# Kernel optimization log

Hardware: AMD Instinct MI355X
Metric: run time of the kernel (lower is better)

Reference implementation:

```python
import jax, jax.numpy as jnp
import numpy as np

N, E, IN, ED, H, C, G, NC = 50000, 800000, 128, 32, 4, 16, 64, 2
HC = H * C  # 64
NEG_SLOPE = 0.2
EPS = 1e-5


def _layernorm(x, g, b):
    mu = jnp.mean(x, axis=-1, keepdims=True)
    var = jnp.mean((x - mu) ** 2, axis=-1, keepdims=True)
    return (x - mu) * jax.lax.rsqrt(var + EPS) * g + b


def _gat(x, src, dst, edge_attr, W, a_src, a_dst, We, a_edge, b):
    """PyG GATConv (v1) with edge features, concat=True."""
    n = x.shape[0]
    h, c = a_src.shape
    xw = (x @ W).reshape(n, h, c)                       # [N,H,C]
    al_src = jnp.sum(xw * a_src, axis=-1)               # [N,H]
    al_dst = jnp.sum(xw * a_dst, axis=-1)               # [N,H]
    ew = (edge_attr @ We).reshape(-1, h, c)             # [Ef,H,C]
    al_e = jnp.sum(ew * a_edge, axis=-1)                # [Ef,H]
    alpha = al_src[src] + al_dst[dst] + al_e            # [Ef,H]
    alpha = jnp.where(alpha > 0, alpha, NEG_SLOPE * alpha)
    # segment softmax over incoming edges of each dst node
    amax = jax.ops.segment_max(alpha, dst, num_segments=n)
    amax = jnp.where(jnp.isfinite(amax), amax, 0.0)
    ex = jnp.exp(alpha - amax[dst])
    denom = jax.ops.segment_sum(ex, dst, num_segments=n)
    att = ex / (denom[dst] + 1e-16)                     # [Ef,H]
    msg = xw[src] * att[:, :, None]                     # [Ef,H,C]
    out = jax.ops.segment_sum(msg, dst, num_segments=n) # [N,H,C]
    return out.reshape(n, h * c) + b


def setup_inputs() -> dict:
    ks = jax.random.split(jax.random.key(0), 24)
    s = 0.1
    inp = {
        "x": jax.random.normal(ks[0], (N, IN), jnp.float32),
        "edge_attr": jax.random.normal(ks[1], (E, ED), jnp.float32),
        "W1": jax.random.normal(ks[2], (IN, HC), jnp.float32) * s,
        "as1": jax.random.normal(ks[3], (H, C), jnp.float32) * s,
        "ad1": jax.random.normal(ks[4], (H, C), jnp.float32) * s,
        "We1": jax.random.normal(ks[5], (ED, HC), jnp.float32) * s,
        "ae1": jax.random.normal(ks[6], (H, C), jnp.float32) * s,
        "b1": jnp.zeros((HC,), jnp.float32),
        "W2": jax.random.normal(ks[7], (HC, HC), jnp.float32) * s,
        "as2": jax.random.normal(ks[8], (H, C), jnp.float32) * s,
        "ad2": jax.random.normal(ks[9], (H, C), jnp.float32) * s,
        "We2": jax.random.normal(ks[10], (ED, HC), jnp.float32) * s,
        "ae2": jax.random.normal(ks[11], (H, C), jnp.float32) * s,
        "b2": jnp.zeros((HC,), jnp.float32),
        "g1": jnp.ones((HC,), jnp.float32),
        "be1": jnp.zeros((HC,), jnp.float32),
        "fw1": jax.random.normal(ks[12], (HC, 32), jnp.float32) * s,
        "fb1": jnp.zeros((32,), jnp.float32),
        "g2": jnp.ones((32,), jnp.float32),
        "be2": jnp.zeros((32,), jnp.float32),
        "fw2": jax.random.normal(ks[13], (32, NC), jnp.float32) * s,
        "fb2": jnp.zeros((NC,), jnp.float32),
        "edge_index": jax.random.randint(ks[14], (2, E), 0, N, jnp.int64),
        "batch": jnp.sort(jax.random.randint(ks[15], (N,), 0, G, jnp.int64)),
    }
    return inp


def reference(x, edge_attr, W1, as1, ad1, We1, ae1, b1, W2, as2, ad2, We2, ae2,
              b2, g1, be1, fw1, fb1, g2, be2, fw2, fb2, edge_index, batch):
    src, dst = edge_index[0], edge_index[1]
    e = edge_attr.shape[0]
    # add_self_loops with fill_value='mean' (mean of incoming edge_attr per node)
    cnt = jax.ops.segment_sum(jnp.ones((e,), x.dtype), dst, num_segments=N)
    loop_ea = jax.ops.segment_sum(edge_attr, dst, num_segments=N) / jnp.clip(cnt, 1.0)[:, None]
    ar = jnp.arange(N)
    src_f = jnp.concatenate([src, ar])
    dst_f = jnp.concatenate([dst, ar])
    ea_f = jnp.concatenate([edge_attr, loop_ea], axis=0)

    h = _gat(x, src_f, dst_f, ea_f, W1, as1, ad1, We1, ae1, b1)
    h = jax.nn.relu(h)
    h = _layernorm(h, g1, be1)
    h = _gat(h, src_f, dst_f, ea_f, W2, as2, ad2, We2, ae2, b2)
    h = jax.nn.relu(h)
    pooled = jax.ops.segment_max(h, batch, num_segments=G)   # global_max_pool
    pooled = jnp.where(jnp.isfinite(pooled), pooled, 0.0)
    z = pooled @ fw1 + fb1
    z = _layernorm(z, g2, be2)
    z = jax.nn.relu(z)
    # dropout(p=0.4) is identity in eval mode
    z = z @ fw2 + fb2
    return jax.nn.log_softmax(z, axis=1)
```

## Files before the change

### kernel.cpp

```cpp
#include <hip/hip_runtime.h>
#include <math.h>

#define N_NODES 50000
#define N_EDGES 800000
#define IN_DIM 128
#define ED_DIM 32
#define NH 4
#define CH 16
#define HC 64
#define NG 64
#define NCL 2
#define NEG_SLOPE 0.2f
#define LN_EPS 1e-5f
#define NBLK1 196
#define NB_TILE 3125
#define NB_ECH 3125

__global__ void k_scan_local(const int* __restrict__ cnt, int* __restrict__ tmp_ex,
                             int* __restrict__ bsum) {
    __shared__ int sd[256];
    int t = threadIdx.x, idx = blockIdx.x * 256 + t;
    int v = (idx < N_NODES) ? cnt[idx] : 0;
    sd[t] = v; __syncthreads();
    for (int off = 1; off < 256; off <<= 1) {
        int add = (t >= off) ? sd[t - off] : 0;
        __syncthreads();
        sd[t] += add;
        __syncthreads();
    }
    if (idx < N_NODES) tmp_ex[idx] = sd[t] - v;
    if (t == 255) bsum[blockIdx.x] = sd[t];
}

__global__ __launch_bounds__(256) void k_phase1(
        const float* __restrict__ X, const float* __restrict__ W,
        const float* __restrict__ AS, const float* __restrict__ AD,
        float* __restrict__ XW, float* __restrict__ ALS, float* __restrict__ ALD,
        const float* __restrict__ ea,
        const float* __restrict__ We1, const float* __restrict__ ae1,
        const float* __restrict__ We2, const float* __restrict__ ae2,
        float4* __restrict__ ale8,
        const int* __restrict__ dst, int* __restrict__ cnt, int* __restrict__ rank_e) {
    __shared__ float smem[IN_DIM * HC + 16 * IN_DIM];
    int job = blockIdx.x % 3;
    int bid = blockIdx.x / 3;
    int t = threadIdx.x;
    if (job == 0) {
        const int K = IN_DIM;
        float* sW = smem;
        float* sX = smem + K * HC;
        for (int i = t; i < K * HC; i += 256) sW[i] = W[i];
        int nb = bid * 16;
        for (int i = t; i < 16 * K; i += 256) sX[i] = X[(long long)nb * K + i];
        __syncthreads();
        int sub = t >> 6, j = t & 63;
        float acc[4] = {0.f, 0.f, 0.f, 0.f};
        #pragma unroll 8
        for (int k = 0; k < K; ++k) {
            float wv = sW[k * HC + j];
            #pragma unroll
            for (int q = 0; q < 4; ++q) acc[q] += sX[(sub + 4 * q) * K + k] * wv;
        }
        float as_ = AS[j], ad_ = AD[j];
        #pragma unroll
        for (int q = 0; q < 4; ++q) {
            int n = nb + sub + 4 * q;
            XW[(long long)n * HC + j] = acc[q];
            float vs = acc[q] * as_, vd = acc[q] * ad_;
            #pragma unroll
            for (int m = 1; m < 16; m <<= 1) { vs += __shfl_xor(vs, m); vd += __shfl_xor(vd, m); }
            if ((j & 15) == 0) {
                int h = j >> 4;
                ALS[n * 4 + h] = vs; ALD[n * 4 + h] = vd;
            }
        }
    } else if (job == 1) {
        float* sVe = smem;
        {
            int d = t >> 3, k = t & 7;
            int l = k >> 2, h = k & 3;
            const float* We = l ? We2 : We1;
            const float* ae = l ? ae2 : ae1;
            float s = 0.f;
            #pragma unroll
            for (int c = 0; c < CH; ++c) s += We[d * HC + h * CH + c] * ae[h * CH + c];
            sVe[d * 8 + k] = s;
        }
        __syncthreads();
        int e = bid * 256 + t;
        if (e >= N_EDGES) return;
        float a[8];
        #pragma unroll
        for (int k = 0; k < 8; ++k) a[k] = 0.f;
        const float4* er4 = (const float4*)(ea + (long long)e * ED_DIM);
        #pragma unroll
        for (int q = 0; q < ED_DIM / 4; ++q) {
            float4 v = er4[q];
            float ev[4] = {v.x, v.y, v.z, v.w};
            #pragma unroll
            for (int u = 0; u < 4; ++u) {
                #pragma unroll
                for (int k = 0; k < 8; ++k) a[k] += ev[u] * sVe[(q * 4 + u) * 8 + k];
            }
        }
        float4* out = ale8 + (long long)e * 2;
        out[0] = make_float4(a[0], a[1], a[2], a[3]);
        out[1] = make_float4(a[4], a[5], a[6], a[7]);
    } else {
        int e = bid * 256 + t;
        if (e < N_EDGES) rank_e[e] = atomicAdd(&cnt[dst[e]], 1);
    }
}

__global__ void k_scan_perm(const int* __restrict__ tmp_ex, const int* __restrict__ bsum,
                            int* __restrict__ row_start,
                            const int* __restrict__ dst, const int* __restrict__ srcI,
                            const int* __restrict__ rank_e, int2* __restrict__ perm_src) {
    __shared__ int sd[256];
    __shared__ int sboff[256];
    int t = threadIdx.x;
    int v = (t < NBLK1) ? bsum[t] : 0;
    sd[t] = v; __syncthreads();
    for (int off = 1; off < 256; off <<= 1) {
        int add = (t >= off) ? sd[t - off] : 0;
        __syncthreads();
        sd[t] += add;
        __syncthreads();
    }
    sboff[t] = sd[t] - v;
    __syncthreads();
    if (blockIdx.x < NBLK1) {
        int idx = blockIdx.x * 256 + t;
        if (idx < N_NODES) row_start[idx] = tmp_ex[idx] + sboff[blockIdx.x];
        if (idx == 0) row_start[N_NODES] = N_EDGES;
    } else {
        int e = (blockIdx.x - NBLK1) * 256 + t;
        if (e < N_EDGES) {
            int d = dst[e];
            int pos = tmp_ex[d] + sboff[d >> 8] + rank_e[e];
            perm_src[pos] = make_int2(e, srcI[e]);
        }
    }
}

template<int K>
__global__ void k_xw(const float* __restrict__ X, const float* __restrict__ W,
                     const float* __restrict__ AS, const float* __restrict__ AD,
                     float* __restrict__ XW, float* __restrict__ ALS, float* __restrict__ ALD) {
    __shared__ float sW[K * HC];
    __shared__ float sX[16 * K];
    int t = threadIdx.x;
    for (int i = t; i < K * HC; i += 256) sW[i] = W[i];
    int nb = blockIdx.x * 16;
    for (int i = t; i < 16 * K; i += 256) sX[i] = X[(long long)nb * K + i];
    __syncthreads();
    int sub = t >> 6, j = t & 63;
    float acc[4] = {0.f, 0.f, 0.f, 0.f};
    #pragma unroll 8
    for (int k = 0; k < K; ++k) {
        float wv = sW[k * HC + j];
        #pragma unroll
        for (int q = 0; q < 4; ++q) acc[q] += sX[(sub + 4 * q) * K + k] * wv;
    }
    float as_ = AS[j], ad_ = AD[j];
    #pragma unroll
    for (int q = 0; q < 4; ++q) {
        int n = nb + sub + 4 * q;
        XW[(long long)n * HC + j] = acc[q];
        float vs = acc[q] * as_, vd = acc[q] * ad_;
        #pragma unroll
        for (int m = 1; m < 16; m <<= 1) { vs += __shfl_xor(vs, m); vd += __shfl_xor(vd, m); }
        if ((j & 15) == 0) {
            int h = j >> 4;
            ALS[n * 4 + h] = vs; ALD[n * 4 + h] = vd;
        }
    }
}

template<bool DO_LN, int LOFF>
__global__ void k_agg(const int* __restrict__ rs, const int2* __restrict__ ps,
                      const float* __restrict__ ale8,
                      const float* __restrict__ ALS, const float* __restrict__ ALD,
                      const float* __restrict__ XW, const float* __restrict__ bias,
                      const float* __restrict__ gam, const float* __restrict__ bet,
                      float* __restrict__ OUT) {
    int n = (blockIdx.x * blockDim.x + threadIdx.x) >> 6;
    if (n >= N_NODES) return;
    int lane = threadIdx.x & 63;
    int h = lane >> 4;
    int e0 = rs[n], e1 = rs[n + 1];
    float adn = ALD[n * 4 + h];
    float acc0 = 0.f, l0 = 0.f, as0 = 0.f;
    float acc1 = 0.f, l1 = 0.f, as1 = 0.f;
    float acc2 = 0.f, l2 = 0.f, as2 = 0.f;
    float acc3 = 0.f, l3 = 0.f, as3 = 0.f;
    int e = e0;
    for (; e + 3 < e1; e += 4) {
        int2 pA = ps[e], pB = ps[e + 1], pC = ps[e + 2], pD = ps[e + 3];
        float aeA = ale8[(long long)pA.x * 8 + LOFF + h];
        float aeB = ale8[(long long)pB.x * 8 + LOFF + h];
        float aeC = ale8[(long long)pC.x * 8 + LOFF + h];
        float aeD = ale8[(long long)pD.x * 8 + LOFF + h];
        float xA = XW[pA.y * HC + lane];
        float xB = XW[pB.y * HC + lane];
        float xC = XW[pC.y * HC + lane];
        float xD = XW[pD.y * HC + lane];
        float aA = ALS[pA.y * 4 + h] + adn + aeA;
        float aB = ALS[pB.y * 4 + h] + adn + aeB;
        float aC = ALS[pC.y * 4 + h] + adn + aeC;
        float aD = ALS[pD.y * 4 + h] + adn + aeD;
        aA = aA > 0.f ? aA : NEG_SLOPE * aA;
        aB = aB > 0.f ? aB : NEG_SLOPE * aB;
        aC = aC > 0.f ? aC : NEG_SLOPE * aC;
        aD = aD > 0.f ? aD : NEG_SLOPE * aD;
        float qA = __expf(aA), qB = __expf(aB), qC = __expf(aC), qD = __expf(aD);
        acc0 += qA * xA; l0 += qA; as0 += aeA;
        acc1 += qB * xB; l1 += qB; as1 += aeB;
        acc2 += qC * xC; l2 += qC; as2 += aeC;
        acc3 += qD * xD; l3 += qD; as3 += aeD;
    }
    for (; e < e1; ++e) {
        int2 pA = ps[e];
        float aeA = ale8[(long long)pA.x * 8 + LOFF + h];
        float xA = XW[pA.y * HC + lane];
        float aA = ALS[pA.y * 4 + h] + adn + aeA;
        aA = aA > 0.f ? aA : NEG_SLOPE * aA;
        float qA = __expf(aA);
        acc0 += qA * xA; l0 += qA; as0 += aeA;
    }
    int d = e1 - e0;
    float invd = 1.f / (float)(d > 0 ? d : 1);
    float aSelf = ALS[n * 4 + h] + adn + (as0 + as1 + as2 + as3) * invd;
    aSelf = aSelf > 0.f ? aSelf : NEG_SLOPE * aSelf;
    float pS = __expf(aSelf);
    float acc = (acc0 + acc1) + (acc2 + acc3) + pS * XW[n * HC + lane];
    float l = (l0 + l1) + (l2 + l3) + pS;
    float v = acc / (l + 1e-16f) + bias[lane];
    v = fmaxf(v, 0.f);
    if (DO_LN) {
        float s1 = v;
        #pragma unroll
        for (int mm = 1; mm < 64; mm <<= 1) s1 += __shfl_xor(s1, mm);
        float mean = s1 * (1.f / 64.f);
        float dd = v - mean;
        float s2 = dd * dd;
        #pragma unroll
        for (int mm = 1; mm < 64; mm <<= 1) s2 += __shfl_xor(s2, mm);
        float var = s2 * (1.f / 64.f);
        v = dd * rsqrtf(var + LN_EPS) * gam[lane] + bet[lane];
    }
    OUT[(long long)n * HC + lane] = v;
}

__global__ void k_pool(const float* __restrict__ H2, const int* __restrict__ batch,
                       float* __restrict__ pooled) {
    int j = threadIdx.x & 63;
    int r = threadIdx.x >> 6;
    int base = blockIdx.x * 128;
    int gcur = -1; float rm = 0.f;
    for (int n = base + r; n < base + 128 && n < N_NODES; n += 4) {
        int g = batch[n];
        if (g != gcur) {
            if (gcur >= 0) atomicMax((unsigned int*)&pooled[gcur * HC + j], __float_as_uint(rm));
            gcur = g; rm = 0.f;
        }
        rm = fmaxf(rm, H2[(long long)n * HC + j]);
    }
    if (gcur >= 0) atomicMax((unsigned int*)&pooled[gcur * HC + j], __float_as_uint(rm));
}

__global__ void k_head(const float* __restrict__ pooled,
                       const float* __restrict__ fw1, const float* __restrict__ fb1,
                       const float* __restrict__ g2, const float* __restrict__ be2,
                       const float* __restrict__ fw2, const float* __restrict__ fb2,
                       float* __restrict__ out) {
    int g = blockIdx.x;
    int j = threadIdx.x;
    float z = 0.f;
    if (j < 32) {
        for (int k = 0; k < HC; ++k) z += pooled[g * HC + k] * fw1[k * 32 + j];
        z += fb1[j];
    }
    float s1 = (j < 32) ? z : 0.f;
    for (int m = 1; m < 32; m <<= 1) s1 += __shfl_xor(s1, m, 32);
    float mean = s1 * (1.f / 32.f);
    float d = z - mean;
    float s2 = (j < 32) ? d * d : 0.f;
    for (int m = 1; m < 32; m <<= 1) s2 += __shfl_xor(s2, m, 32);
    float var = s2 * (1.f / 32.f);
    float zz = 0.f;
    if (j < 32) {
        zz = d * rsqrtf(var + LN_EPS) * g2[j] + be2[j];
        zz = fmaxf(zz, 0.f);
    }
    float p0 = (j < 32) ? zz * fw2[j * NCL + 0] : 0.f;
    float p1 = (j < 32) ? zz * fw2[j * NCL + 1] : 0.f;
    for (int m = 1; m < 32; m <<= 1) { p0 += __shfl_xor(p0, m, 32); p1 += __shfl_xor(p1, m, 32); }
    if (j == 0) {
        float l0 = p0 + fb2[0], l1 = p1 + fb2[1];
        float mx = fmaxf(l0, l1);
        float ls = mx + logf(__expf(l0 - mx) + __expf(l1 - mx));
        out[g * NCL + 0] = l0 - ls;
        out[g * NCL + 1] = l1 - ls;
    }
}

extern "C" void kernel_launch(void* const* d_in, const int* in_sizes, int n_in,
                              void* d_out, int out_size, void* d_ws, size_t ws_size,
                              hipStream_t stream) {
    const float* x   = (const float*)d_in[0];
    const float* ea  = (const float*)d_in[1];
    const float* W1  = (const float*)d_in[2];
    const float* as1 = (const float*)d_in[3];
    const float* ad1 = (const float*)d_in[4];
    const float* We1 = (const float*)d_in[5];
    const float* ae1 = (const float*)d_in[6];
    const float* b1  = (const float*)d_in[7];
    const float* W2  = (const float*)d_in[8];
    const float* as2 = (const float*)d_in[9];
    const float* ad2 = (const float*)d_in[10];
    const float* We2 = (const float*)d_in[11];
    const float* ae2 = (const float*)d_in[12];
    const float* b2  = (const float*)d_in[13];
    const float* g1  = (const float*)d_in[14];
    const float* be1 = (const float*)d_in[15];
    const float* fw1 = (const float*)d_in[16];
    const float* fb1 = (const float*)d_in[17];
    const float* g2  = (const float*)d_in[18];
    const float* be2 = (const float*)d_in[19];
    const float* fw2 = (const float*)d_in[20];
    const float* fb2 = (const float*)d_in[21];
    const int* eidx  = (const int*)d_in[22];
    const int* batch = (const int*)d_in[23];
    const int* srcI = eidx;
    const int* dstI = eidx + N_EDGES;

    char* w = (char*)d_ws;
    auto alloc = [&](size_t bytes) { char* p = w; w += (bytes + 255) & ~(size_t)255; return p; };
    int*   cnt       = (int*)  alloc((size_t)N_NODES * 4);
    int*   row_start = (int*)  alloc((size_t)(N_NODES + 1) * 4);
    int*   rank_e    = (int*)  alloc((size_t)N_EDGES * 4);
    int*   tmp_ex    = (int*)  alloc((size_t)N_NODES * 4);
    int*   bsum      = (int*)  alloc(256 * 4);
    int2*  perm_src  = (int2*) alloc((size_t)N_EDGES * 8);
    float4* ale8     = (float4*)alloc((size_t)N_EDGES * 32);
    float* xw1       = (float*)alloc((size_t)N_NODES * HC * 4);
    float* als1      = (float*)alloc((size_t)N_NODES * 4 * 4);
    float* ald1      = (float*)alloc((size_t)N_NODES * 4 * 4);
    float* h1        = (float*)alloc((size_t)N_NODES * HC * 4);
    float* als2      = (float*)alloc((size_t)N_NODES * 4 * 4);
    float* ald2      = (float*)alloc((size_t)N_NODES * 4 * 4);
    float* pooled    = (float*)alloc((size_t)NG * HC * 4);
    float* xw2 = xw1;
    float* h2  = h1;

    hipMemsetAsync(cnt, 0, (size_t)N_NODES * 4, stream);
    hipMemsetAsync(pooled, 0, (size_t)NG * HC * 4, stream);

    k_phase1<<<3 * NB_TILE, 256, 0, stream>>>(x, W1, as1, ad1, xw1, als1, ald1,
                                              ea, We1, ae1, We2, ae2, ale8,
                                              dstI, cnt, rank_e);
    k_scan_local<<<NBLK1, 256, 0, stream>>>(cnt, tmp_ex, bsum);
    k_scan_perm<<<NBLK1 + NB_ECH, 256, 0, stream>>>(tmp_ex, bsum, row_start,
                                                    dstI, srcI, rank_e, perm_src);

    k_agg<true, 0><<<N_NODES / 4, 256, 0, stream>>>(row_start, perm_src, (const float*)ale8,
                                                    als1, ald1, xw1, b1, g1, be1, h1);
    k_xw<HC><<<N_NODES / 16, 256, 0, stream>>>(h1, W2, as2, ad2, xw2, als2, ald2);
    k_agg<false, 4><<<N_NODES / 4, 256, 0, stream>>>(row_start, perm_src, (const float*)ale8,
                                                     als2, ald2, xw2, b2, nullptr, nullptr, h2);

    k_pool<<<(N_NODES + 127) / 128, 256, 0, stream>>>(h2, batch, pooled);
    k_head<<<NG, 64, 0, stream>>>(pooled, fw1, fb1, g2, be2, fw2, fb2, (float*)d_out);
}
```

Measured before the change: 418.6 us.

## Fuse layer-2 projection into layer-1 aggregation and pooling into layer-2 aggregation

The layer-1 aggregation kernel now applies LayerNorm, stages the normalized row in shared memory and multiplies it by W2 in place, writing XW2 and the layer-2 attention logits directly. The separate h1 buffer and k_xw launch go away. The layer-2 aggregation then does global max pooling itself with per-node atomicMax into pooled, which removes the h2 write/read and the k_pool launch. In exchange it issues many more atomics, one per node and lane instead of one per run of nodes, and W2 is read from global/L1 per node instead of from a shared tile.

```diff
diff --git a/kernel.cpp b/kernel.cpp
--- a/kernel.cpp
+++ b/kernel.cpp
@@ -143,47 +143,17 @@
     }
 }
 
-template<int K>
-__global__ void k_xw(const float* __restrict__ X, const float* __restrict__ W,
-                     const float* __restrict__ AS, const float* __restrict__ AD,
-                     float* __restrict__ XW, float* __restrict__ ALS, float* __restrict__ ALD) {
-    __shared__ float sW[K * HC];
-    __shared__ float sX[16 * K];
-    int t = threadIdx.x;
-    for (int i = t; i < K * HC; i += 256) sW[i] = W[i];
-    int nb = blockIdx.x * 16;
-    for (int i = t; i < 16 * K; i += 256) sX[i] = X[(long long)nb * K + i];
-    __syncthreads();
-    int sub = t >> 6, j = t & 63;
-    float acc[4] = {0.f, 0.f, 0.f, 0.f};
-    #pragma unroll 8
-    for (int k = 0; k < K; ++k) {
-        float wv = sW[k * HC + j];
-        #pragma unroll
-        for (int q = 0; q < 4; ++q) acc[q] += sX[(sub + 4 * q) * K + k] * wv;
-    }
-    float as_ = AS[j], ad_ = AD[j];
-    #pragma unroll
-    for (int q = 0; q < 4; ++q) {
-        int n = nb + sub + 4 * q;
-        XW[(long long)n * HC + j] = acc[q];
-        float vs = acc[q] * as_, vd = acc[q] * ad_;
-        #pragma unroll
-        for (int m = 1; m < 16; m <<= 1) { vs += __shfl_xor(vs, m); vd += __shfl_xor(vd, m); }
-        if ((j & 15) == 0) {
-            int h = j >> 4;
-            ALS[n * 4 + h] = vs; ALD[n * 4 + h] = vd;
-        }
-    }
-}
-
-template<bool DO_LN, int LOFF>
-__global__ void k_agg(const int* __restrict__ rs, const int2* __restrict__ ps,
-                      const float* __restrict__ ale8,
-                      const float* __restrict__ ALS, const float* __restrict__ ALD,
-                      const float* __restrict__ XW, const float* __restrict__ bias,
-                      const float* __restrict__ gam, const float* __restrict__ bet,
-                      float* __restrict__ OUT) {
+__global__ void k_agg1x(const int* __restrict__ rs, const int2* __restrict__ ps,
+                        const float* __restrict__ ale8,
+                        const float* __restrict__ ALS, const float* __restrict__ ALD,
+                        const float* __restrict__ XW, const float* __restrict__ bias,
+                        const float* __restrict__ gam, const float* __restrict__ bet,
+                        const float* __restrict__ W2,
+                        const float* __restrict__ AS2, const float* __restrict__ AD2,
+                        float* __restrict__ XW2, float* __restrict__ ALS2,
+                        float* __restrict__ ALD2) {
+    __shared__ float sh[4][HC];
+    int wid = threadIdx.x >> 6;
     int n = (blockIdx.x * blockDim.x + threadIdx.x) >> 6;
     if (n >= N_NODES) return;
     int lane = threadIdx.x & 63;
@@ -197,10 +167,10 @@
     int e = e0;
     for (; e + 3 < e1; e += 4) {
         int2 pA = ps[e], pB = ps[e + 1], pC = ps[e + 2], pD = ps[e + 3];
-        float aeA = ale8[(long long)pA.x * 8 + LOFF + h];
-        float aeB = ale8[(long long)pB.x * 8 + LOFF + h];
-        float aeC = ale8[(long long)pC.x * 8 + LOFF + h];
-        float aeD = ale8[(long long)pD.x * 8 + LOFF + h];
+        float aeA = ale8[(long long)pA.x * 8 + h];
+        float aeB = ale8[(long long)pB.x * 8 + h];
+        float aeC = ale8[(long long)pC.x * 8 + h];
+        float aeD = ale8[(long long)pD.x * 8 + h];
         float xA = XW[pA.y * HC + lane];
         float xB = XW[pB.y * HC + lane];
         float xC = XW[pC.y * HC + lane];
@@ -221,7 +191,7 @@
     }
     for (; e < e1; ++e) {
         int2 pA = ps[e];
-        float aeA = ale8[(long long)pA.x * 8 + LOFF + h];
+        float aeA = ale8[(long long)pA.x * 8 + h];
         float xA = XW[pA.y * HC + lane];
         float aA = ALS[pA.y * 4 + h] + adn + aeA;
         aA = aA > 0.f ? aA : NEG_SLOPE * aA;
@@ -237,7 +207,7 @@
     float l = (l0 + l1) + (l2 + l3) + pS;
     float v = acc / (l + 1e-16f) + bias[lane];
     v = fmaxf(v, 0.f);
-    if (DO_LN) {
+    {
         float s1 = v;
         #pragma unroll
         for (int mm = 1; mm < 64; mm <<= 1) s1 += __shfl_xor(s1, mm);
@@ -249,24 +219,82 @@
         float var = s2 * (1.f / 64.f);
         v = dd * rsqrtf(var + LN_EPS) * gam[lane] + bet[lane];
     }
-    OUT[(long long)n * HC + lane] = v;
-}
-
-__global__ void k_pool(const float* __restrict__ H2, const int* __restrict__ batch,
-                       float* __restrict__ pooled) {
-    int j = threadIdx.x & 63;
-    int r = threadIdx.x >> 6;
-    int base = blockIdx.x * 128;
-    int gcur = -1; float rm = 0.f;
-    for (int n = base + r; n < base + 128 && n < N_NODES; n += 4) {
-        int g = batch[n];
-        if (g != gcur) {
-            if (gcur >= 0) atomicMax((unsigned int*)&pooled[gcur * HC + j], __float_as_uint(rm));
-            gcur = g; rm = 0.f;
-        }
-        rm = fmaxf(rm, H2[(long long)n * HC + j]);
-    }
-    if (gcur >= 0) atomicMax((unsigned int*)&pooled[gcur * HC + j], __float_as_uint(rm));
+    sh[wid][lane] = v;
+    __syncthreads();
+    float a2 = 0.f;
+    #pragma unroll 8
+    for (int k = 0; k < HC; ++k) {
+        a2 += sh[wid][k] * W2[k * HC + lane];
+    }
+    XW2[(long long)n * HC + lane] = a2;
+    float vs = a2 * AS2[lane], vd = a2 * AD2[lane];
+    #pragma unroll
+    for (int m = 1; m < 16; m <<= 1) { vs += __shfl_xor(vs, m); vd += __shfl_xor(vd, m); }
+    if ((lane & 15) == 0) {
+        ALS2[n * 4 + h] = vs; ALD2[n * 4 + h] = vd;
+    }
+}
+
+__global__ void k_agg2p(const int* __restrict__ rs, const int2* __restrict__ ps,
+                        const float* __restrict__ ale8,
+                        const float* __restrict__ ALS, const float* __restrict__ ALD,
+                        const float* __restrict__ XW, const float* __restrict__ bias,
+                        const int* __restrict__ batch, float* __restrict__ pooled) {
+    int n = (blockIdx.x * blockDim.x + threadIdx.x) >> 6;
+    if (n >= N_NODES) return;
+    int lane = threadIdx.x & 63;
+    int h = lane >> 4;
+    int e0 = rs[n], e1 = rs[n + 1];
+    float adn = ALD[n * 4 + h];
+    float acc0 = 0.f, l0 = 0.f, as0 = 0.f;
+    float acc1 = 0.f, l1 = 0.f, as1 = 0.f;
+    float acc2 = 0.f, l2 = 0.f, as2 = 0.f;
+    float acc3 = 0.f, l3 = 0.f, as3 = 0.f;
+    int e = e0;
+    for (; e + 3 < e1; e += 4) {
+        int2 pA = ps[e], pB = ps[e + 1], pC = ps[e + 2], pD = ps[e + 3];
+        float aeA = ale8[(long long)pA.x * 8 + 4 + h];
+        float aeB = ale8[(long long)pB.x * 8 + 4 + h];
+        float aeC = ale8[(long long)pC.x * 8 + 4 + h];
+        float aeD = ale8[(long long)pD.x * 8 + 4 + h];
+        float xA = XW[pA.y * HC + lane];
+        float xB = XW[pB.y * HC + lane];
+        float xC = XW[pC.y * HC + lane];
+        float xD = XW[pD.y * HC + lane];
+        float aA = ALS[pA.y * 4 + h] + adn + aeA;
+        float aB = ALS[pB.y * 4 + h] + adn + aeB;
+        float aC = ALS[pC.y * 4 + h] + adn + aeC;
+        float aD = ALS[pD.y * 4 + h] + adn + aeD;
+        aA = aA > 0.f ? aA : NEG_SLOPE * aA;
+        aB = aB > 0.f ? aB : NEG_SLOPE * aB;
+        aC = aC > 0.f ? aC : NEG_SLOPE * aC;
+        aD = aD > 0.f ? aD : NEG_SLOPE * aD;
+        float qA = __expf(aA), qB = __expf(aB), qC = __expf(aC), qD = __expf(aD);
+        acc0 += qA * xA; l0 += qA; as0 += aeA;
+        acc1 += qB * xB; l1 += qB; as1 += aeB;
+        acc2 += qC * xC; l2 += qC; as2 += aeC;
+        acc3 += qD * xD; l3 += qD; as3 += aeD;
+    }
+    for (; e < e1; ++e) {
+        int2 pA = ps[e];
+        float aeA = ale8[(long long)pA.x * 8 + 4 + h];
+        float xA = XW[pA.y * HC + lane];
+        float aA = ALS[pA.y * 4 + h] + adn + aeA;
+        aA = aA > 0.f ? aA : NEG_SLOPE * aA;
+        float qA = __expf(aA);
+        acc0 += qA * xA; l0 += qA; as0 += aeA;
+    }
+    int d = e1 - e0;
+    float invd = 1.f / (float)(d > 0 ? d : 1);
+    float aSelf = ALS[n * 4 + h] + adn + (as0 + as1 + as2 + as3) * invd;
+    aSelf = aSelf > 0.f ? aSelf : NEG_SLOPE * aSelf;
+    float pS = __expf(aSelf);
+    float acc = (acc0 + acc1) + (acc2 + acc3) + pS * XW[n * HC + lane];
+    float l = (l0 + l1) + (l2 + l3) + pS;
+    float v = acc / (l + 1e-16f) + bias[lane];
+    v = fmaxf(v, 0.f);
+    int g = batch[n];
+    atomicMax((unsigned int*)&pooled[g * HC + lane], __float_as_uint(v));
 }
 
 __global__ void k_head(const float* __restrict__ pooled,
@@ -347,12 +375,10 @@
     float* xw1       = (float*)alloc((size_t)N_NODES * HC * 4);
     float* als1      = (float*)alloc((size_t)N_NODES * 4 * 4);
     float* ald1      = (float*)alloc((size_t)N_NODES * 4 * 4);
-    float* h1        = (float*)alloc((size_t)N_NODES * HC * 4);
+    float* xw2       = (float*)alloc((size_t)N_NODES * HC * 4);
     float* als2      = (float*)alloc((size_t)N_NODES * 4 * 4);
     float* ald2      = (float*)alloc((size_t)N_NODES * 4 * 4);
     float* pooled    = (float*)alloc((size_t)NG * HC * 4);
-    float* xw2 = xw1;
-    float* h2  = h1;
 
     hipMemsetAsync(cnt, 0, (size_t)N_NODES * 4, stream);
     hipMemsetAsync(pooled, 0, (size_t)NG * HC * 4, stream);
@@ -364,12 +390,11 @@
     k_scan_perm<<<NBLK1 + NB_ECH, 256, 0, stream>>>(tmp_ex, bsum, row_start,
                                                     dstI, srcI, rank_e, perm_src);
 
-    k_agg<true, 0><<<N_NODES / 4, 256, 0, stream>>>(row_start, perm_src, (const float*)ale8,
-                                                    als1, ald1, xw1, b1, g1, be1, h1);
-    k_xw<HC><<<N_NODES / 16, 256, 0, stream>>>(h1, W2, as2, ad2, xw2, als2, ald2);
-    k_agg<false, 4><<<N_NODES / 4, 256, 0, stream>>>(row_start, perm_src, (const float*)ale8,
-                                                     als2, ald2, xw2, b2, nullptr, nullptr, h2);
-
-    k_pool<<<(N_NODES + 127) / 128, 256, 0, stream>>>(h2, batch, pooled);
+    k_agg1x<<<N_NODES / 4, 256, 0, stream>>>(row_start, perm_src, (const float*)ale8,
+                                             als1, ald1, xw1, b1, g1, be1,
+                                             W2, as2, ad2, xw2, als2, ald2);
+    k_agg2p<<<N_NODES / 4, 256, 0, stream>>>(row_start, perm_src, (const float*)ale8,
+                                             als2, ald2, xw2, b2, batch, pooled);
+
     k_head<<<NG, 64, 0, stream>>>(pooled, fw1, fb1, g2, be2, fw2, fb2, (float*)d_out);
 }
```

Measured after the change: 435.4 us. 1.04x slower.

## Pack source attention logits beside XW rows and use persistent aggregation waves

Applied to the files above, without the earlier changes.

Stores each node's per-head source attention logit in a padded 68-float row right after its 64 XW features. Each gathered edge then reads its features and logit from the same row, where before it touched a separate ALS array. The aggregation kernels also change to a grid-stride loop over a fixed 2048 blocks instead of one wave per node, which cuts launch and wave scheduling overhead. The cost is a larger, non-power-of-two row stride that may misalign rows against cache lines, and persistent waves can load-balance worse across skewed degree distributions.

```diff
diff --git a/kernel.cpp b/kernel.cpp
--- a/kernel.cpp
+++ b/kernel.cpp
@@ -8,6 +8,7 @@
 #define NH 4
 #define CH 16
 #define HC 64
+#define XS 68
 #define NG 64
 #define NCL 2
 #define NEG_SLOPE 0.2f
@@ -15,6 +16,8 @@
 #define NBLK1 196
 #define NB_TILE 3125
 #define NB_ECH 3125
+#define AGG_BLOCKS 2048
+#define AGG_WAVES (AGG_BLOCKS * 4)
 
 __global__ void k_scan_local(const int* __restrict__ cnt, int* __restrict__ tmp_ex,
                              int* __restrict__ bsum) {
@@ -35,7 +38,7 @@
 __global__ __launch_bounds__(256) void k_phase1(
         const float* __restrict__ X, const float* __restrict__ W,
         const float* __restrict__ AS, const float* __restrict__ AD,
-        float* __restrict__ XW, float* __restrict__ ALS, float* __restrict__ ALD,
+        float* __restrict__ XWA, float* __restrict__ ALD,
         const float* __restrict__ ea,
         const float* __restrict__ We1, const float* __restrict__ ae1,
         const float* __restrict__ We2, const float* __restrict__ ae2,
@@ -65,13 +68,14 @@
         #pragma unroll
         for (int q = 0; q < 4; ++q) {
             int n = nb + sub + 4 * q;
-            XW[(long long)n * HC + j] = acc[q];
+            XWA[(long long)n * XS + j] = acc[q];
             float vs = acc[q] * as_, vd = acc[q] * ad_;
             #pragma unroll
             for (int m = 1; m < 16; m <<= 1) { vs += __shfl_xor(vs, m); vd += __shfl_xor(vd, m); }
             if ((j & 15) == 0) {
                 int h = j >> 4;
-                ALS[n * 4 + h] = vs; ALD[n * 4 + h] = vd;
+                XWA[(long long)n * XS + 64 + h] = vs;
+                ALD[n * 4 + h] = vd;
             }
         }
     } else if (job == 1) {
@@ -146,7 +150,7 @@
 template<int K>
 __global__ void k_xw(const float* __restrict__ X, const float* __restrict__ W,
                      const float* __restrict__ AS, const float* __restrict__ AD,
-                     float* __restrict__ XW, float* __restrict__ ALS, float* __restrict__ ALD) {
+                     float* __restrict__ XWA, float* __restrict__ ALD) {
     __shared__ float sW[K * HC];
     __shared__ float sX[16 * K];
     int t = threadIdx.x;
@@ -166,13 +170,14 @@
     #pragma unroll
     for (int q = 0; q < 4; ++q) {
         int n = nb + sub + 4 * q;
-        XW[(long long)n * HC + j] = acc[q];
+        XWA[(long long)n * XS + j] = acc[q];
         float vs = acc[q] * as_, vd = acc[q] * ad_;
         #pragma unroll
         for (int m = 1; m < 16; m <<= 1) { vs += __shfl_xor(vs, m); vd += __shfl_xor(vd, m); }
         if ((j & 15) == 0) {
             int h = j >> 4;
-            ALS[n * 4 + h] = vs; ALD[n * 4 + h] = vd;
+            XWA[(long long)n * XS + 64 + h] = vs;
+            ALD[n * 4 + h] = vd;
         }
     }
 }
@@ -180,76 +185,77 @@
 template<bool DO_LN, int LOFF>
 __global__ void k_agg(const int* __restrict__ rs, const int2* __restrict__ ps,
                       const float* __restrict__ ale8,
-                      const float* __restrict__ ALS, const float* __restrict__ ALD,
-                      const float* __restrict__ XW, const float* __restrict__ bias,
+                      const float* __restrict__ XWA, const float* __restrict__ ALD,
+                      const float* __restrict__ bias,
                       const float* __restrict__ gam, const float* __restrict__ bet,
                       float* __restrict__ OUT) {
-    int n = (blockIdx.x * blockDim.x + threadIdx.x) >> 6;
-    if (n >= N_NODES) return;
+    int gw = (blockIdx.x * blockDim.x + threadIdx.x) >> 6;
     int lane = threadIdx.x & 63;
     int h = lane >> 4;
-    int e0 = rs[n], e1 = rs[n + 1];
-    float adn = ALD[n * 4 + h];
-    float acc0 = 0.f, l0 = 0.f, as0 = 0.f;
-    float acc1 = 0.f, l1 = 0.f, as1 = 0.f;
-    float acc2 = 0.f, l2 = 0.f, as2 = 0.f;
-    float acc3 = 0.f, l3 = 0.f, as3 = 0.f;
-    int e = e0;
-    for (; e + 3 < e1; e += 4) {
-        int2 pA = ps[e], pB = ps[e + 1], pC = ps[e + 2], pD = ps[e + 3];
-        float aeA = ale8[(long long)pA.x * 8 + LOFF + h];
-        float aeB = ale8[(long long)pB.x * 8 + LOFF + h];
-        float aeC = ale8[(long long)pC.x * 8 + LOFF + h];
-        float aeD = ale8[(long long)pD.x * 8 + LOFF + h];
-        float xA = XW[pA.y * HC + lane];
-        float xB = XW[pB.y * HC + lane];
-        float xC = XW[pC.y * HC + lane];
-        float xD = XW[pD.y * HC + lane];
-        float aA = ALS[pA.y * 4 + h] + adn + aeA;
-        float aB = ALS[pB.y * 4 + h] + adn + aeB;
-        float aC = ALS[pC.y * 4 + h] + adn + aeC;
-        float aD = ALS[pD.y * 4 + h] + adn + aeD;
-        aA = aA > 0.f ? aA : NEG_SLOPE * aA;
-        aB = aB > 0.f ? aB : NEG_SLOPE * aB;
-        aC = aC > 0.f ? aC : NEG_SLOPE * aC;
-        aD = aD > 0.f ? aD : NEG_SLOPE * aD;
-        float qA = __expf(aA), qB = __expf(aB), qC = __expf(aC), qD = __expf(aD);
-        acc0 += qA * xA; l0 += qA; as0 += aeA;
-        acc1 += qB * xB; l1 += qB; as1 += aeB;
-        acc2 += qC * xC; l2 += qC; as2 += aeC;
-        acc3 += qD * xD; l3 += qD; as3 += aeD;
-    }
-    for (; e < e1; ++e) {
-        int2 pA = ps[e];
-        float aeA = ale8[(long long)pA.x * 8 + LOFF + h];
-        float xA = XW[pA.y * HC + lane];
-        float aA = ALS[pA.y * 4 + h] + adn + aeA;
-        aA = aA > 0.f ? aA : NEG_SLOPE * aA;
-        float qA = __expf(aA);
-        acc0 += qA * xA; l0 += qA; as0 += aeA;
-    }
-    int d = e1 - e0;
-    float invd = 1.f / (float)(d > 0 ? d : 1);
-    float aSelf = ALS[n * 4 + h] + adn + (as0 + as1 + as2 + as3) * invd;
-    aSelf = aSelf > 0.f ? aSelf : NEG_SLOPE * aSelf;
-    float pS = __expf(aSelf);
-    float acc = (acc0 + acc1) + (acc2 + acc3) + pS * XW[n * HC + lane];
-    float l = (l0 + l1) + (l2 + l3) + pS;
-    float v = acc / (l + 1e-16f) + bias[lane];
-    v = fmaxf(v, 0.f);
-    if (DO_LN) {
-        float s1 = v;
-        #pragma unroll
-        for (int mm = 1; mm < 64; mm <<= 1) s1 += __shfl_xor(s1, mm);
-        float mean = s1 * (1.f / 64.f);
-        float dd = v - mean;
-        float s2 = dd * dd;
-        #pragma unroll
-        for (int mm = 1; mm < 64; mm <<= 1) s2 += __shfl_xor(s2, mm);
-        float var = s2 * (1.f / 64.f);
-        v = dd * rsqrtf(var + LN_EPS) * gam[lane] + bet[lane];
-    }
-    OUT[(long long)n * HC + lane] = v;
+    for (int n = gw; n < N_NODES; n += AGG_WAVES) {
+        int e0 = rs[n], e1 = rs[n + 1];
+        float adn = ALD[n * 4 + h];
+        float acc0 = 0.f, l0 = 0.f, as0 = 0.f;
+        float acc1 = 0.f, l1 = 0.f, as1 = 0.f;
+        float acc2 = 0.f, l2 = 0.f, as2 = 0.f;
+        float acc3 = 0.f, l3 = 0.f, as3 = 0.f;
+        int e = e0;
+        for (; e + 3 < e1; e += 4) {
+            int2 pA = ps[e], pB = ps[e + 1], pC = ps[e + 2], pD = ps[e + 3];
+            float aeA = ale8[(long long)pA.x * 8 + LOFF + h];
+            float aeB = ale8[(long long)pB.x * 8 + LOFF + h];
+            float aeC = ale8[(long long)pC.x * 8 + LOFF + h];
+            float aeD = ale8[(long long)pD.x * 8 + LOFF + h];
+            float xA = XWA[(long long)pA.y * XS + lane];
+            float xB = XWA[(long long)pB.y * XS + lane];
+            float xC = XWA[(long long)pC.y * XS + lane];
+            float xD = XWA[(long long)pD.y * XS + lane];
+            float aA = XWA[(long long)pA.y * XS + 64 + h] + adn + aeA;
+            float aB = XWA[(long long)pB.y * XS + 64 + h] + adn + aeB;
+            float aC = XWA[(long long)pC.y * XS + 64 + h] + adn + aeC;
+            float aD = XWA[(long long)pD.y * XS + 64 + h] + adn + aeD;
+            aA = aA > 0.f ? aA : NEG_SLOPE * aA;
+            aB = aB > 0.f ? aB : NEG_SLOPE * aB;
+            aC = aC > 0.f ? aC : NEG_SLOPE * aC;
+            aD = aD > 0.f ? aD : NEG_SLOPE * aD;
+            float qA = __expf(aA), qB = __expf(aB), qC = __expf(aC), qD = __expf(aD);
+            acc0 += qA * xA; l0 += qA; as0 += aeA;
+            acc1 += qB * xB; l1 += qB; as1 += aeB;
+            acc2 += qC * xC; l2 += qC; as2 += aeC;
+            acc3 += qD * xD; l3 += qD; as3 += aeD;
+        }
+        for (; e < e1; ++e) {
+            int2 pA = ps[e];
+            float aeA = ale8[(long long)pA.x * 8 + LOFF + h];
+            float xA = XWA[(long long)pA.y * XS + lane];
+            float aA = XWA[(long long)pA.y * XS + 64 + h] + adn + aeA;
+            aA = aA > 0.f ? aA : NEG_SLOPE * aA;
+            float qA = __expf(aA);
+            acc0 += qA * xA; l0 += qA; as0 += aeA;
+        }
+        int d = e1 - e0;
+        float invd = 1.f / (float)(d > 0 ? d : 1);
+        float aSelf = XWA[(long long)n * XS + 64 + h] + adn + (as0 + as1 + as2 + as3) * invd;
+        aSelf = aSelf > 0.f ? aSelf : NEG_SLOPE * aSelf;
+        float pS = __expf(aSelf);
+        float acc = (acc0 + acc1) + (acc2 + acc3) + pS * XWA[(long long)n * XS + lane];
+        float l = (l0 + l1) + (l2 + l3) + pS;
+        float v = acc / (l + 1e-16f) + bias[lane];
+        v = fmaxf(v, 0.f);
+        if (DO_LN) {
+            float s1 = v;
+            #pragma unroll
+            for (int mm = 1; mm < 64; mm <<= 1) s1 += __shfl_xor(s1, mm);
+            float mean = s1 * (1.f / 64.f);
+            float dd = v - mean;
+            float s2 = dd * dd;
+            #pragma unroll
+            for (int mm = 1; mm < 64; mm <<= 1) s2 += __shfl_xor(s2, mm);
+            float var = s2 * (1.f / 64.f);
+            v = dd * rsqrtf(var + LN_EPS) * gam[lane] + bet[lane];
+        }
+        OUT[(long long)n * HC + lane] = v;
+    }
 }
 
 __global__ void k_pool(const float* __restrict__ H2, const int* __restrict__ batch,
@@ -344,31 +350,29 @@
     int*   bsum      = (int*)  alloc(256 * 4);
     int2*  perm_src  = (int2*) alloc((size_t)N_EDGES * 8);
     float4* ale8     = (float4*)alloc((size_t)N_EDGES * 32);
-    float* xw1       = (float*)alloc((size_t)N_NODES * HC * 4);
-    float* als1      = (float*)alloc((size_t)N_NODES * 4 * 4);
+    float* xwa1      = (float*)alloc((size_t)N_NODES * XS * 4);
     float* ald1      = (float*)alloc((size_t)N_NODES * 4 * 4);
     float* h1        = (float*)alloc((size_t)N_NODES * HC * 4);
-    float* als2      = (float*)alloc((size_t)N_NODES * 4 * 4);
     float* ald2      = (float*)alloc((size_t)N_NODES * 4 * 4);
     float* pooled    = (float*)alloc((size_t)NG * HC * 4);
-    float* xw2 = xw1;
+    float* xwa2 = xwa1;
     float* h2  = h1;
 
     hipMemsetAsync(cnt, 0, (size_t)N_NODES * 4, stream);
     hipMemsetAsync(pooled, 0, (size_t)NG * HC * 4, stream);
 
-    k_phase1<<<3 * NB_TILE, 256, 0, stream>>>(x, W1, as1, ad1, xw1, als1, ald1,
+    k_phase1<<<3 * NB_TILE, 256, 0, stream>>>(x, W1, as1, ad1, xwa1, ald1,
                                               ea, We1, ae1, We2, ae2, ale8,
                                               dstI, cnt, rank_e);
     k_scan_local<<<NBLK1, 256, 0, stream>>>(cnt, tmp_ex, bsum);
     k_scan_perm<<<NBLK1 + NB_ECH, 256, 0, stream>>>(tmp_ex, bsum, row_start,
                                                     dstI, srcI, rank_e, perm_src);
 
-    k_agg<true, 0><<<N_NODES / 4, 256, 0, stream>>>(row_start, perm_src, (const float*)ale8,
-                                                    als1, ald1, xw1, b1, g1, be1, h1);
-    k_xw<HC><<<N_NODES / 16, 256, 0, stream>>>(h1, W2, as2, ad2, xw2, als2, ald2);
-    k_agg<false, 4><<<N_NODES / 4, 256, 0, stream>>>(row_start, perm_src, (const float*)ale8,
-                                                     als2, ald2, xw2, b2, nullptr, nullptr, h2);
+    k_agg<true, 0><<<AGG_BLOCKS, 256, 0, stream>>>(row_start, perm_src, (const float*)ale8,
+                                                   xwa1, ald1, b1, g1, be1, h1);
+    k_xw<HC><<<NB_TILE, 256, 0, stream>>>(h1, W2, as2, ad2, xwa2, ald2);
+    k_agg<false, 4><<<AGG_BLOCKS, 256, 0, stream>>>(row_start, perm_src, (const float*)ale8,
+                                                    xwa2, ald2, b2, nullptr, nullptr, h2);
 
     k_pool<<<(N_NODES + 127) / 128, 256, 0, stream>>>(h2, batch, pooled);
     k_head<<<NG, 64, 0, stream>>>(pooled, fw1, fb1, g2, be2, fw2, fb2, (float*)d_out);
```

Result: slower. 451.3 us (+7.8%).
